# Kernel optimization log

Measured on AMD Instinct MI355X. Metric: run time of the kernel, lower is better.

Reference implementation:

```python
import jax, jax.numpy as jnp
import numpy as np

B = 16384
OUT = 128          # output_size (per conditioning frame)
NCOND = 3
HID = 32           # MLP3 hidden
LSTM_H = 64        # lstm_output_size (input == hidden)
NPRED = 25
EPS = 1e-5


def setup_inputs() -> dict:
    key = jax.random.key(0)
    ks = jax.random.split(key, 20)
    d = {
        "x0": jax.random.normal(ks[0], (B, OUT), jnp.float32),
        "x1": jax.random.normal(ks[1], (B, OUT), jnp.float32),
        "x2": jax.random.normal(ks[2], (B, OUT), jnp.float32),
        # MLP3: Linear(384->32), BN, ReLU, Linear(32->32), BN, ReLU, Linear(32->64)
        "W1": jax.random.normal(ks[3], (HID, OUT * NCOND), jnp.float32) * 0.05,
        "b1": jnp.full((HID,), 0.03, jnp.float32),
        "g1": jnp.ones((HID,), jnp.float32),
        "beta1": jnp.zeros((HID,), jnp.float32),
        "W2": jax.random.normal(ks[4], (HID, HID), jnp.float32) * 0.1,
        "b2": jnp.full((HID,), 0.03, jnp.float32),
        "g2": jnp.ones((HID,), jnp.float32),
        "beta2": jnp.zeros((HID,), jnp.float32),
        "W3": jax.random.normal(ks[5], (LSTM_H, HID), jnp.float32) * 0.1,
        "b3": jnp.full((LSTM_H,), 0.03, jnp.float32),
        # LSTM (torch gate order i,f,g,o): weight_ih (4H,H), weight_hh (4H,H)
        "Wih": jax.random.normal(ks[6], (4 * LSTM_H, LSTM_H), jnp.float32) * 0.08,
        "Whh": jax.random.normal(ks[7], (4 * LSTM_H, LSTM_H), jnp.float32) * 0.08,
        "bih": jnp.zeros((4 * LSTM_H,), jnp.float32),
        "bhh": jnp.zeros((4 * LSTM_H,), jnp.float32),
    }
    return d


def _bn_train(h, g, b):
    # BatchNorm1d in training mode: biased batch statistics
    m = jnp.mean(h, axis=0)
    v = jnp.var(h, axis=0)
    return g * (h - m) * jax.lax.rsqrt(v + EPS) + b


def _lstm_step(inp, h, c, Wih, Whh, bih, bhh):
    gates = inp @ Wih.T + bih + h @ Whh.T + bhh  # (B, 4H)
    i, f, g, o = jnp.split(gates, 4, axis=1)
    c_new = jax.nn.sigmoid(f) * c + jax.nn.sigmoid(i) * jnp.tanh(g)
    h_new = jax.nn.sigmoid(o) * jnp.tanh(c_new)
    return h_new, c_new


def reference(x0, x1, x2, W1, b1, g1, beta1, W2, b2, g2, beta2, W3, b3,
              Wih, Whh, bih, bhh):
    x = jnp.concatenate([x0, x1, x2], axis=1)          # (B, 384)
    h = jax.nn.relu(_bn_train(x @ W1.T + b1, g1, beta1))
    h = jax.nn.relu(_bn_train(h @ W2.T + b2, g2, beta2))
    m = h @ W3.T + b3                                   # (B, 64)

    h0 = jnp.zeros((m.shape[0], LSTM_H), m.dtype)
    c0 = jnp.zeros_like(h0)
    # initial conditioning step (output discarded except as state/next input)
    h1, c1 = _lstm_step(m, h0, c0, Wih, Whh, bih, bhh)

    def step(carry, _):
        hh, cc = carry
        # loop feeds previous output back as input; output == h for 1-layer LSTM
        hn, cn = _lstm_step(hh, hh, cc, Wih, Whh, bih, bhh)
        return (hn, cn), hn

    _, outs = jax.lax.scan(step, (h1, c1), None, length=NPRED)  # (25, B, 64)
    return jnp.transpose(outs, (1, 0, 2))                        # (B, 25, 64)
```

## Files before the change

kernel.cpp:

```cpp
#include <hip/hip_runtime.h>


#define EPSV 1e-5f
#define LOG2E 1.4426950408889634f
#define K2    2.8853900817779268f

typedef __attribute__((ext_vector_type(8))) short bf16x8;
typedef __attribute__((ext_vector_type(4))) float f32x4;

__device__ __forceinline__ float rcp_f(float x) { return __builtin_amdgcn_rcpf(x); }
__device__ __forceinline__ void split_bf16(float x, ushort& hi, ushort& lo) {
    unsigned xb = __builtin_bit_cast(unsigned, x);
    hi = (ushort)(xb >> 16);
    float hif = __builtin_bit_cast(float, xb & 0xffff0000u);
    unsigned lb = __builtin_bit_cast(unsigned, x - hif);
    lo = (ushort)(lb >> 16);
}
__device__ __forceinline__ void split8(const float* w, bf16x8& hiv, bf16x8& lov) {
    ushort hs[8], ls[8];
    #pragma unroll
    for (int j = 0; j < 8; ++j) split_bf16(w[j], hs[j], ls[j]);
    hiv = *(bf16x8*)hs;
    lov = *(bf16x8*)ls;
}

__global__ __launch_bounds__(256) void k_red(
    const float* __restrict__ part, const float* __restrict__ g,
    const float* __restrict__ be, float* __restrict__ scsh,
    int do_prep,
    const float* __restrict__ Wih, const float* __restrict__ Whh,
    const float* __restrict__ bih, const float* __restrict__ bhh,
    ushort* __restrict__ Wih_hi, ushort* __restrict__ Wih_lo,
    ushort* __restrict__ Wsum_hi, ushort* __restrict__ Wsum_lo,
    float* __restrict__ bsum)
{
    __shared__ float rs[256], rq[256];
    const int ch = blockIdx.x, t = threadIdx.x;

    if (do_prep) {
        #pragma unroll
        for (int e = 0; e < 2; ++e) {
            int i = blockIdx.x * 512 + e * 256 + t;
            int j = i >> 6;
            float sc = (j >= 128 && j < 192) ? K2 : LOG2E;
            float wi  = Wih[i] * sc;
            float wsv = (Wih[i] + Whh[i]) * sc;
            ushort h, l;
            split_bf16(wi, h, l);  Wih_hi[i] = h;  Wih_lo[i] = l;
            split_bf16(wsv, h, l); Wsum_hi[i] = h; Wsum_lo[i] = l;
        }
        if (blockIdx.x == 0) {
            float sc = (t >= 128 && t < 192) ? K2 : LOG2E;
            bsum[t] = (bih[t] + bhh[t]) * sc;
        }
    }

    float s = (part[t * 32 + ch] + part[(t + 256) * 32 + ch]) +
              (part[(t + 512) * 32 + ch] + part[(t + 768) * 32 + ch]);
    float q = (part[32768 + t * 32 + ch] + part[32768 + (t + 256) * 32 + ch]) +
              (part[32768 + (t + 512) * 32 + ch] + part[32768 + (t + 768) * 32 + ch]);
    rs[t] = s; rq[t] = q;
    __syncthreads();
    #pragma unroll
    for (int off = 128; off > 0; off >>= 1) {
        if (t < off) { rs[t] += rs[t + off]; rq[t] += rq[t + off]; }
        __syncthreads();
    }
    if (t == 0) {
        float mu = rs[0] * (1.f / 16384.f);
        float va = rq[0] * (1.f / 16384.f) - mu * mu;
        float sc = g[ch] * rsqrtf(va + EPSV);
        scsh[ch] = sc; scsh[32 + ch] = be[ch] - mu * sc;
    }
}

__global__ __launch_bounds__(256, 2) void k_mlp1(
    const float* __restrict__ x0, const float* __restrict__ x1, const float* __restrict__ x2,
    const float* __restrict__ W1, const float* __restrict__ b1,
    float* __restrict__ pre, float* __restrict__ st1p)
{
    __shared__ __align__(16) ushort xhi[32 * 392];
    __shared__ __align__(16) ushort xlo[32 * 392];
    const int tid = threadIdx.x;
    const int r0  = blockIdx.x * 32;
    const int lane = tid & 63, l15 = lane & 15, lg = lane >> 4, q = tid >> 6;
    const int m0 = (q & 1) * 16, n0 = (q >> 1) * 16;

    bf16x8 WH[12], WL[12];
    {
        const float* wsrc = W1 + (size_t)(n0 + l15) * 384 + lg * 8;
        #pragma unroll
        for (int kt = 0; kt < 12; ++kt) {
            float w[8];
            float4 wa = *(const float4*)(wsrc + kt * 32);
            float4 wb = *(const float4*)(wsrc + kt * 32 + 4);
            w[0] = wa.x; w[1] = wa.y; w[2] = wa.z; w[3] = wa.w;
            w[4] = wb.x; w[5] = wb.y; w[6] = wb.z; w[7] = wb.w;
            split8(w, WH[kt], WL[kt]);
        }
    }

    for (int a = 0; a < 3; ++a) {
        const float* xp = (a == 0) ? x0 : (a == 1) ? x1 : x2;
        const float4* src = (const float4*)(xp + (size_t)r0 * 128);
        #pragma unroll
        for (int it = 0; it < 4; ++it) {
            int i = it * 256 + tid;
            int row = i >> 5, c4 = i & 31;
            float4 v = src[i];
            ushort h0, l0, h1, l1, h2, l2, h3, l3;
            split_bf16(v.x, h0, l0); split_bf16(v.y, h1, l1);
            split_bf16(v.z, h2, l2); split_bf16(v.w, h3, l3);
            int ofs = row * 392 + a * 128 + c4 * 4;
            *(ushort4*)&xhi[ofs] = make_ushort4(h0, h1, h2, h3);
            *(ushort4*)&xlo[ofs] = make_ushort4(l0, l1, l2, l3);
        }
    }
    __syncthreads();

    const float bias = b1[n0 + l15];
    f32x4 acc = {bias, bias, bias, bias};
    #pragma unroll
    for (int kt = 0; kt < 12; ++kt) {
        bf16x8 ahi = *(const bf16x8*)&xhi[(m0 + l15) * 392 + kt * 32 + lg * 8];
        bf16x8 alo = *(const bf16x8*)&xlo[(m0 + l15) * 392 + kt * 32 + lg * 8];
        acc = __builtin_amdgcn_mfma_f32_16x16x32_bf16(ahi, WH[kt], acc, 0, 0, 0);
        acc = __builtin_amdgcn_mfma_f32_16x16x32_bf16(ahi, WL[kt], acc, 0, 0, 0);
        acc = __builtin_amdgcn_mfma_f32_16x16x32_bf16(alo, WH[kt], acc, 0, 0, 0);
    }
    #pragma unroll
    for (int rg = 0; rg < 4; ++rg)
        pre[(size_t)(r0 + m0 + lg * 4 + rg) * 32 + n0 + l15] = acc[rg];
    float s  = (acc[0] + acc[1]) + (acc[2] + acc[3]);
    float sq = (acc[0] * acc[0] + acc[1] * acc[1]) + (acc[2] * acc[2] + acc[3] * acc[3]);
    s  += __shfl_xor(s, 16);  s  += __shfl_xor(s, 32);
    sq += __shfl_xor(sq, 16); sq += __shfl_xor(sq, 32);
    if (lg == 0) {
        int slot = (blockIdx.x * 2 + (q & 1)) * 32 + n0 + l15;
        st1p[slot] = s;
        st1p[32768 + slot] = sq;
    }
}

__global__ __launch_bounds__(256) void k_mlp2(
    float* __restrict__ pre, const float* __restrict__ scsh1,
    const float* __restrict__ W2, const float* __restrict__ b2,
    float* __restrict__ st2p)
{
    __shared__ __align__(16) ushort hhi[32 * 40];
    __shared__ __align__(16) ushort hlo[32 * 40];
    __shared__ float bnsc[32], bnsh[32];
    const int tid = threadIdx.x;
    const int r0  = blockIdx.x * 32;
    const int lane = tid & 63, l15 = lane & 15, lg = lane >> 4, q = tid >> 6;
    const int m0 = (q & 1) * 16, n0 = (q >> 1) * 16;

    bf16x8 W2H, W2L;
    {
        const float* wsrc = W2 + (size_t)(n0 + l15) * 32 + lg * 8;
        float w[8];
        float4 wa = *(const float4*)(wsrc);
        float4 wb = *(const float4*)(wsrc + 4);
        w[0] = wa.x; w[1] = wa.y; w[2] = wa.z; w[3] = wa.w;
        w[4] = wb.x; w[5] = wb.y; w[6] = wb.z; w[7] = wb.w;
        split8(w, W2H, W2L);
    }

    if (tid < 32) { bnsc[tid] = scsh1[tid]; bnsh[tid] = scsh1[32 + tid]; }
    __syncthreads();
    {
        int row = tid >> 3, c4 = tid & 7;
        float4 v = ((const float4*)(pre + (size_t)r0 * 32))[tid];
        float e0 = fmaxf(fmaf(v.x, bnsc[c4 * 4 + 0], bnsh[c4 * 4 + 0]), 0.f);
        float e1 = fmaxf(fmaf(v.y, bnsc[c4 * 4 + 1], bnsh[c4 * 4 + 1]), 0.f);
        float e2 = fmaxf(fmaf(v.z, bnsc[c4 * 4 + 2], bnsh[c4 * 4 + 2]), 0.f);
        float e3 = fmaxf(fmaf(v.w, bnsc[c4 * 4 + 3], bnsh[c4 * 4 + 3]), 0.f);
        ushort h0, l0, h1, l1, h2, l2, h3, l3;
        split_bf16(e0, h0, l0); split_bf16(e1, h1, l1);
        split_bf16(e2, h2, l2); split_bf16(e3, h3, l3);
        int ofs = row * 40 + c4 * 4;
        *(ushort4*)&hhi[ofs] = make_ushort4(h0, h1, h2, h3);
        *(ushort4*)&hlo[ofs] = make_ushort4(l0, l1, l2, l3);
    }
    __syncthreads();

    const float bias = b2[n0 + l15];
    f32x4 acc = {bias, bias, bias, bias};
    bf16x8 ahi = *(const bf16x8*)&hhi[(m0 + l15) * 40 + lg * 8];
    bf16x8 alo = *(const bf16x8*)&hlo[(m0 + l15) * 40 + lg * 8];
    acc = __builtin_amdgcn_mfma_f32_16x16x32_bf16(ahi, W2H, acc, 0, 0, 0);
    acc = __builtin_amdgcn_mfma_f32_16x16x32_bf16(ahi, W2L, acc, 0, 0, 0);
    acc = __builtin_amdgcn_mfma_f32_16x16x32_bf16(alo, W2H, acc, 0, 0, 0);

    #pragma unroll
    for (int rg = 0; rg < 4; ++rg)
        pre[(size_t)(r0 + m0 + lg * 4 + rg) * 32 + n0 + l15] = acc[rg];
    float s  = (acc[0] + acc[1]) + (acc[2] + acc[3]);
    float sq = (acc[0] * acc[0] + acc[1] * acc[1]) + (acc[2] * acc[2] + acc[3] * acc[3]);
    s  += __shfl_xor(s, 16);  s  += __shfl_xor(s, 32);
    sq += __shfl_xor(sq, 16); sq += __shfl_xor(sq, 32);
    if (lg == 0) {
        int slot = (blockIdx.x * 2 + (q & 1)) * 32 + n0 + l15;
        st2p[slot] = s;
        st2p[32768 + slot] = sq;
    }
}

__global__ __launch_bounds__(256, 2) void k_lstm(
    const float* __restrict__ pre, const float* __restrict__ scsh2,
    const float* __restrict__ W3, const float* __restrict__ b3,
    const ushort* __restrict__ Wih_hi, const ushort* __restrict__ Wih_lo,
    const ushort* __restrict__ Wsum_hi, const ushort* __restrict__ Wsum_lo,
    const float* __restrict__ bsum, float* __restrict__ out)
{
    __shared__ __align__(16) ushort hhi[2][2][16][72];
    __shared__ __align__(16) ushort hlo[2][2][16][72];
    __shared__ float bn2sc[32], bn2sh[32];
    const int tid  = threadIdx.x;
    const int lane = tid & 63, l15 = lane & 15, lg = lane >> 4, q = tid >> 6;
    const int r0   = blockIdx.x * 32;

    if (tid < 32) { bn2sc[tid] = scsh2[tid]; bn2sh[tid] = scsh2[32 + tid]; }
    __syncthreads();

    {
        const int row = tid & 31, seg = tid >> 5;
        float h2[32];
        const float4* pr = (const float4*)(pre + (size_t)(r0 + row) * 32);
        #pragma unroll
        for (int j4 = 0; j4 < 8; ++j4) {
            float4 v = pr[j4];
            h2[j4 * 4 + 0] = v.x; h2[j4 * 4 + 1] = v.y;
            h2[j4 * 4 + 2] = v.z; h2[j4 * 4 + 3] = v.w;
        }
        #pragma unroll
        for (int j = 0; j < 32; ++j) h2[j] = fmaxf(fmaf(h2[j], bn2sc[j], bn2sh[j]), 0.f);
        #pragma unroll
        for (int uu = 0; uu < 8; ++uu) {
            int u = seg * 8 + uu;
            const float* w = W3 + u * 32;
            float a0 = 0.f, a1 = 0.f, a2 = 0.f, a3 = 0.f;
            #pragma unroll
            for (int k = 0; k < 32; k += 4) {
                a0 = fmaf(h2[k + 0], w[k + 0], a0);
                a1 = fmaf(h2[k + 1], w[k + 1], a1);
                a2 = fmaf(h2[k + 2], w[k + 2], a2);
                a3 = fmaf(h2[k + 3], w[k + 3], a3);
            }
            float m = b3[u] + ((a0 + a1) + (a2 + a3));
            ushort mh, ml; split_bf16(m, mh, ml);
            hhi[row >> 4][0][row & 15][u] = mh;
            hlo[row >> 4][0][row & 15][u] = ml;
        }
    }

    float bias[4];
    #pragma unroll
    for (int nt = 0; nt < 4; ++nt) bias[nt] = bsum[nt * 64 + q * 16 + l15];
    float cA[4] = {0.f, 0.f, 0.f, 0.f}, cB[4] = {0.f, 0.f, 0.f, 0.f};

    float* obA[4];
    float* obB[4];
    #pragma unroll
    for (int rg = 0; rg < 4; ++rg) {
        obA[rg] = out + (size_t)(r0 + lg * 4 + rg) * 1600 + (q * 16 + l15);
        obB[rg] = out + (size_t)(r0 + 16 + lg * 4 + rg) * 1600 + (q * 16 + l15);
    }

    bf16x8 Bhi[4][2], Blo[4][2];
    const size_t wofs = (size_t)(q * 16 + l15) * 64 + lg * 8;
    #pragma unroll
    for (int nt = 0; nt < 4; ++nt)
        #pragma unroll
        for (int kt = 0; kt < 2; ++kt) {
            Bhi[nt][kt] = *(const bf16x8*)(Wih_hi + (size_t)nt * 4096 + wofs + kt * 32);
            Blo[nt][kt] = *(const bf16x8*)(Wih_lo + (size_t)nt * 4096 + wofs + kt * 32);
        }
    __syncthreads();

    if ((blockIdx.x >> 8) & 1) __builtin_amdgcn_s_sleep(46);

#define MFMA_GATES(ACC, G, BUF)                                                  \
    {                                                                            \
        _Pragma("unroll")                                                        \
        for (int nt = 0; nt < 4; ++nt)                                           \
            ACC[nt] = (f32x4){bias[nt], bias[nt], bias[nt], bias[nt]};           \
        _Pragma("unroll")                                                        \
        for (int kt = 0; kt < 2; ++kt) {                                         \
            bf16x8 ahi = *(const bf16x8*)&hhi[G][BUF][l15][kt * 32 + lg * 8];    \
            bf16x8 alo = *(const bf16x8*)&hlo[G][BUF][l15][kt * 32 + lg * 8];    \
            _Pragma("unroll")                                                    \
            for (int nt = 0; nt < 4; ++nt) {                                     \
                ACC[nt] = __builtin_amdgcn_mfma_f32_16x16x32_bf16(ahi, Bhi[nt][kt], ACC[nt], 0, 0, 0); \
                ACC[nt] = __builtin_amdgcn_mfma_f32_16x16x32_bf16(ahi, Blo[nt][kt], ACC[nt], 0, 0, 0); \
                ACC[nt] = __builtin_amdgcn_mfma_f32_16x16x32_bf16(alo, Bhi[nt][kt], ACC[nt], 0, 0, 0); \
            }                                                                    \
        }                                                                        \
    }

#define ACT(ACC, C, G, WBUF, OB, SLOT, WRST)                                     \
    {                                                                            \
        const int u = q * 16 + l15;                                              \
        _Pragma("unroll")                                                        \
        for (int rg = 0; rg < 4; ++rg) {                                         \
            int row = lg * 4 + rg;                                               \
            float iv = ACC[0][rg], fv = ACC[1][rg];                              \
            float gv = ACC[2][rg], ov = ACC[3][rg];                              \
            float Af = __builtin_amdgcn_exp2f(-fv);                              \
            float Ai = __builtin_amdgcn_exp2f(-iv);                              \
            float Bg = __builtin_amdgcn_exp2f(gv);                               \
            float sig = (Bg - 1.f) * rcp_f((1.f + Ai) * (Bg + 1.f));             \
            float cc = C[rg] * rcp_f(1.f + Af) + sig;                            \
            C[rg] = cc;                                                          \
            float Ao = __builtin_amdgcn_exp2f(-ov);                              \
            float C2 = __builtin_amdgcn_exp2f(cc * K2);                          \
            float hn = (C2 - 1.f) * rcp_f((1.f + Ao) * (C2 + 1.f));              \
            ushort hh, hl; split_bf16(hn, hh, hl);                               \
            hhi[G][WBUF][row][u] = hh;                                           \
            hlo[G][WBUF][row][u] = hl;                                           \
            if (WRST)                                                            \
                OB[rg][(size_t)(SLOT) * 64] = hn;                                \
        }                                                                        \
    }

    f32x4 accA[4], accB[4];

    MFMA_GATES(accA, 0, 0);
    MFMA_GATES(accB, 1, 0);
    #pragma unroll
    for (int nt = 0; nt < 4; ++nt)
        #pragma unroll
        for (int kt = 0; kt < 2; ++kt) {
            Bhi[nt][kt] = *(const bf16x8*)(Wsum_hi + (size_t)nt * 4096 + wofs + kt * 32);
            Blo[nt][kt] = *(const bf16x8*)(Wsum_lo + (size_t)nt * 4096 + wofs + kt * 32);
        }
    ACT(accA, cA, 0, 1, obA, 0, 0);
    ACT(accB, cB, 1, 1, obB, 0, 0);
    __syncthreads();

    #pragma unroll 1
    for (int s = 1; s <= 25; ++s) {
        const int rb = s & 1, wb = rb ^ 1;
        MFMA_GATES(accA, 0, rb);
        MFMA_GATES(accB, 1, rb);
        ACT(accA, cA, 0, wb, obA, s - 1, 1);
        ACT(accB, cB, 1, wb, obB, s - 1, 1);
        __syncthreads();
    }

#undef MFMA_GATES
#undef ACT
}

extern "C" void kernel_launch(void* const* d_in, const int* in_sizes, int n_in,
                              void* d_out, int out_size, void* d_ws, size_t ws_size,
                              hipStream_t stream) {
    const float* x0   = (const float*)d_in[0];
    const float* x1   = (const float*)d_in[1];
    const float* x2   = (const float*)d_in[2];
    const float* W1   = (const float*)d_in[3];
    const float* b1   = (const float*)d_in[4];
    const float* g1   = (const float*)d_in[5];
    const float* be1  = (const float*)d_in[6];
    const float* W2   = (const float*)d_in[7];
    const float* b2   = (const float*)d_in[8];
    const float* g2   = (const float*)d_in[9];
    const float* be2  = (const float*)d_in[10];
    const float* W3   = (const float*)d_in[11];
    const float* b3   = (const float*)d_in[12];
    const float* Wih  = (const float*)d_in[13];
    const float* Whh  = (const float*)d_in[14];
    const float* bih  = (const float*)d_in[15];
    const float* bhh  = (const float*)d_in[16];

    float* ws    = (float*)d_ws;
    float* pre   = ws;
    float* st1p  = ws + 524288;
    float* st2p  = ws + 589824;
    float* scsh1 = ws + 655360;
    float* scsh2 = ws + 655424;
    float* bsum  = ws + 655488;
    ushort* ub   = (ushort*)(ws + 655744);
    ushort* Wih_hi  = ub;
    ushort* Wih_lo  = ub + 16384;
    ushort* Wsum_hi = ub + 32768;
    ushort* Wsum_lo = ub + 49152;

    hipLaunchKernelGGL(k_mlp1, dim3(512), dim3(256), 0, stream,
                       x0, x1, x2, W1, b1, pre, st1p);
    hipLaunchKernelGGL(k_red, dim3(32), dim3(256), 0, stream,
                       st1p, g1, be1, scsh1,
                       1, Wih, Whh, bih, bhh, Wih_hi, Wih_lo, Wsum_hi, Wsum_lo, bsum);
    hipLaunchKernelGGL(k_mlp2, dim3(512), dim3(256), 0, stream,
                       pre, scsh1, W2, b2, st2p);
    hipLaunchKernelGGL(k_red, dim3(32), dim3(256), 0, stream,
                       st2p, g2, be2, scsh2,
                       0, Wih, Whh, bih, bhh, Wih_hi, Wih_lo, Wsum_hi, Wsum_lo, bsum);
    hipLaunchKernelGGL(k_lstm, dim3(512), dim3(256), 0, stream,
                       pre, scsh2, W3, b3,
                       Wih_hi, Wih_lo, Wsum_hi, Wsum_lo, bsum, (float*)d_out);
}
```

Before: 82.08 us.

## Split MFMA accumulation chains, drop staggered sleep, merge LSTM cell reciprocals

```diff
diff --git a/kernel.cpp b/kernel.cpp
--- a/kernel.cpp
+++ b/kernel.cpp
@@ -119,15 +119,23 @@
     __syncthreads();
 
     const float bias = b1[n0 + l15];
-    f32x4 acc = {bias, bias, bias, bias};
+    f32x4 acc  = {bias, bias, bias, bias};
+    f32x4 acc2 = {0.f, 0.f, 0.f, 0.f};
     #pragma unroll
     for (int kt = 0; kt < 12; ++kt) {
         bf16x8 ahi = *(const bf16x8*)&xhi[(m0 + l15) * 392 + kt * 32 + lg * 8];
         bf16x8 alo = *(const bf16x8*)&xlo[(m0 + l15) * 392 + kt * 32 + lg * 8];
-        acc = __builtin_amdgcn_mfma_f32_16x16x32_bf16(ahi, WH[kt], acc, 0, 0, 0);
-        acc = __builtin_amdgcn_mfma_f32_16x16x32_bf16(ahi, WL[kt], acc, 0, 0, 0);
-        acc = __builtin_amdgcn_mfma_f32_16x16x32_bf16(alo, WH[kt], acc, 0, 0, 0);
-    }
+        if (kt & 1) {
+            acc2 = __builtin_amdgcn_mfma_f32_16x16x32_bf16(ahi, WH[kt], acc2, 0, 0, 0);
+            acc2 = __builtin_amdgcn_mfma_f32_16x16x32_bf16(ahi, WL[kt], acc2, 0, 0, 0);
+            acc2 = __builtin_amdgcn_mfma_f32_16x16x32_bf16(alo, WH[kt], acc2, 0, 0, 0);
+        } else {
+            acc = __builtin_amdgcn_mfma_f32_16x16x32_bf16(ahi, WH[kt], acc, 0, 0, 0);
+            acc = __builtin_amdgcn_mfma_f32_16x16x32_bf16(ahi, WL[kt], acc, 0, 0, 0);
+            acc = __builtin_amdgcn_mfma_f32_16x16x32_bf16(alo, WH[kt], acc, 0, 0, 0);
+        }
+    }
+    acc = acc + acc2;
     #pragma unroll
     for (int rg = 0; rg < 4; ++rg)
         pre[(size_t)(r0 + m0 + lg * 4 + rg) * 32 + n0 + l15] = acc[rg];
@@ -149,7 +157,6 @@
 {
     __shared__ __align__(16) ushort hhi[32 * 40];
     __shared__ __align__(16) ushort hlo[32 * 40];
-    __shared__ float bnsc[32], bnsh[32];
     const int tid = threadIdx.x;
     const int r0  = blockIdx.x * 32;
     const int lane = tid & 63, l15 = lane & 15, lg = lane >> 4, q = tid >> 6;
@@ -166,15 +173,15 @@
         split8(w, W2H, W2L);
     }
 
-    if (tid < 32) { bnsc[tid] = scsh1[tid]; bnsh[tid] = scsh1[32 + tid]; }
-    __syncthreads();
     {
         int row = tid >> 3, c4 = tid & 7;
+        float4 scv = *(const float4*)(scsh1 + c4 * 4);
+        float4 shv = *(const float4*)(scsh1 + 32 + c4 * 4);
         float4 v = ((const float4*)(pre + (size_t)r0 * 32))[tid];
-        float e0 = fmaxf(fmaf(v.x, bnsc[c4 * 4 + 0], bnsh[c4 * 4 + 0]), 0.f);
-        float e1 = fmaxf(fmaf(v.y, bnsc[c4 * 4 + 1], bnsh[c4 * 4 + 1]), 0.f);
-        float e2 = fmaxf(fmaf(v.z, bnsc[c4 * 4 + 2], bnsh[c4 * 4 + 2]), 0.f);
-        float e3 = fmaxf(fmaf(v.w, bnsc[c4 * 4 + 3], bnsh[c4 * 4 + 3]), 0.f);
+        float e0 = fmaxf(fmaf(v.x, scv.x, shv.x), 0.f);
+        float e1 = fmaxf(fmaf(v.y, scv.y, shv.y), 0.f);
+        float e2 = fmaxf(fmaf(v.z, scv.z, shv.z), 0.f);
+        float e3 = fmaxf(fmaf(v.w, scv.w, shv.w), 0.f);
         ushort h0, l0, h1, l1, h2, l2, h3, l3;
         split_bf16(e0, h0, l0); split_bf16(e1, h1, l1);
         split_bf16(e2, h2, l2); split_bf16(e3, h3, l3);
@@ -278,24 +285,29 @@
         }
     __syncthreads();
 
-    if ((blockIdx.x >> 8) & 1) __builtin_amdgcn_s_sleep(46);
-
 #define MFMA_GATES(ACC, G, BUF)                                                  \
     {                                                                            \
+        f32x4 _a2[4];                                                            \
         _Pragma("unroll")                                                        \
-        for (int nt = 0; nt < 4; ++nt)                                           \
+        for (int nt = 0; nt < 4; ++nt) {                                         \
             ACC[nt] = (f32x4){bias[nt], bias[nt], bias[nt], bias[nt]};           \
+            _a2[nt] = (f32x4){0.f, 0.f, 0.f, 0.f};                               \
+        }                                                                        \
+        bf16x8 ahi0 = *(const bf16x8*)&hhi[G][BUF][l15][lg * 8];                 \
+        bf16x8 alo0 = *(const bf16x8*)&hlo[G][BUF][l15][lg * 8];                 \
+        bf16x8 ahi1 = *(const bf16x8*)&hhi[G][BUF][l15][32 + lg * 8];            \
+        bf16x8 alo1 = *(const bf16x8*)&hlo[G][BUF][l15][32 + lg * 8];            \
         _Pragma("unroll")                                                        \
-        for (int kt = 0; kt < 2; ++kt) {                                         \
-            bf16x8 ahi = *(const bf16x8*)&hhi[G][BUF][l15][kt * 32 + lg * 8];    \
-            bf16x8 alo = *(const bf16x8*)&hlo[G][BUF][l15][kt * 32 + lg * 8];    \
-            _Pragma("unroll")                                                    \
-            for (int nt = 0; nt < 4; ++nt) {                                     \
-                ACC[nt] = __builtin_amdgcn_mfma_f32_16x16x32_bf16(ahi, Bhi[nt][kt], ACC[nt], 0, 0, 0); \
-                ACC[nt] = __builtin_amdgcn_mfma_f32_16x16x32_bf16(ahi, Blo[nt][kt], ACC[nt], 0, 0, 0); \
-                ACC[nt] = __builtin_amdgcn_mfma_f32_16x16x32_bf16(alo, Bhi[nt][kt], ACC[nt], 0, 0, 0); \
-            }                                                                    \
+        for (int nt = 0; nt < 4; ++nt) {                                         \
+            ACC[nt] = __builtin_amdgcn_mfma_f32_16x16x32_bf16(ahi0, Bhi[nt][0], ACC[nt], 0, 0, 0); \
+            ACC[nt] = __builtin_amdgcn_mfma_f32_16x16x32_bf16(ahi0, Blo[nt][0], ACC[nt], 0, 0, 0); \
+            ACC[nt] = __builtin_amdgcn_mfma_f32_16x16x32_bf16(alo0, Bhi[nt][0], ACC[nt], 0, 0, 0); \
+            _a2[nt] = __builtin_amdgcn_mfma_f32_16x16x32_bf16(ahi1, Bhi[nt][1], _a2[nt], 0, 0, 0); \
+            _a2[nt] = __builtin_amdgcn_mfma_f32_16x16x32_bf16(ahi1, Blo[nt][1], _a2[nt], 0, 0, 0); \
+            _a2[nt] = __builtin_amdgcn_mfma_f32_16x16x32_bf16(alo1, Bhi[nt][1], _a2[nt], 0, 0, 0); \
         }                                                                        \
+        _Pragma("unroll")                                                        \
+        for (int nt = 0; nt < 4; ++nt) ACC[nt] = ACC[nt] + _a2[nt];              \
     }
 
 #define ACT(ACC, C, G, WBUF, OB, SLOT, WRST)                                     \
@@ -309,8 +321,9 @@
             float Af = __builtin_amdgcn_exp2f(-fv);                              \
             float Ai = __builtin_amdgcn_exp2f(-iv);                              \
             float Bg = __builtin_amdgcn_exp2f(gv);                               \
-            float sig = (Bg - 1.f) * rcp_f((1.f + Ai) * (Bg + 1.f));             \
-            float cc = C[rg] * rcp_f(1.f + Af) + sig;                            \
+            float onA = 1.f + Af;                                                \
+            float t   = (1.f + Ai) * (Bg + 1.f);                                 \
+            float cc  = fmaf(C[rg], t, (Bg - 1.f) * onA) * rcp_f(t * onA);       \
             C[rg] = cc;                                                          \
             float Ao = __builtin_amdgcn_exp2f(-ov);                              \
             float C2 = __builtin_amdgcn_exp2f(cc * K2);                          \
```

Measured after the change: 84.82 us. 1.03x slower.
